# Performance work log

Hardware: AMD Instinct MI355X
Metric: run time of the kernel (lower is better)

Reference implementation:

```python
import jax, jax.numpy as jnp
import numpy as np

QMIN, QMAX = 0.0, 255.0  # uint8 activation quantization range


def _qlinear(x, w_q, b, s_in, zp_in, s_w):
    """zentorch_qlinear: quantize fp32 x to uint8, int8 weight, dequant output.

    x:   [M, K] fp32
    w_q: [N, K] int8 values (stored int32), symmetric (weight zp = 0)
    b:   [N] fp32
    s_in, zp_in: scalars (activation scale / zero point)
    s_w: [N] per-output-channel weight scales
    """
    zp = zp_in.astype(jnp.float32)
    q = jnp.clip(jnp.round(x / s_in) + zp, QMIN, QMAX)      # fake-quant uint8
    x_dq = (q - zp) * s_in                                   # dequantized activation
    w_dq = w_q.astype(jnp.float32) * s_w[:, None]            # [N, K] dequant weight
    return x_dq @ w_dq.T + b                                 # [M, N] fp32


def setup_inputs() -> dict:
    key = jax.random.key(0)
    k1, k2, k3, k4 = jax.random.split(key, 4)
    M, K, N = 8192, 4096, 4096
    inp = {
        "input": jax.random.normal(k1, (M, K), dtype=jnp.float32),
        "weights": jax.random.randint(k2, (N, K), -128, 128, dtype=jnp.int32),
        "biases": jax.random.normal(k3, (N,), dtype=jnp.float32) * 0.1,
        "input_scales": jnp.array([0.05], dtype=jnp.float32),
        "input_zero_points": jnp.array([128], dtype=jnp.int32),
        "weight_scales": jax.random.uniform(k4, (N,), dtype=jnp.float32, minval=0.001, maxval=0.01),
        "weight_zero_points": jnp.zeros((N,), dtype=jnp.int32),
        "output_dtype": 0,  # 0 -> float32
    }
    return inp


def reference(input, weights, biases, input_scales, input_zero_points,
              weight_scales, weight_zero_points, output_dtype):
    s_in = input_scales[0]
    zp_in = input_zero_points[0]
    x = _qlinear(input, weights, biases, s_in, zp_in, weight_scales)
    x = _qlinear(x, weights, biases, s_in, zp_in, weight_scales)
    x = _qlinear(x, weights, biases, s_in, zp_in, weight_scales)
    return x
```

## Files before the change

### kernel.cpp

```cpp
#include <hip/hip_runtime.h>
#include <stdint.h>

#define M_DIM 8192
#define K_DIM 4096
#define N_DIM 4096
#define KTILES (K_DIM / 64)

typedef __attribute__((ext_vector_type(4))) int i32x4;

__global__ void pack_w_kernel(const int* __restrict__ w, char* __restrict__ wp,
                              int* __restrict__ corr, const int* __restrict__ zpp) {
  __shared__ int red[256];
  const int n = blockIdx.x;
  const int t = threadIdx.x;
  const int4* row = (const int4*)(w + (size_t)n * K_DIM);
  int s = 0;
  int words[4];
#pragma unroll
  for (int u = 0; u < 4; ++u) {
    int4 v = row[t * 4 + u];
    s += v.x + v.y + v.z + v.w;
    words[u] = (v.x & 255) | ((v.y & 255) << 8) | ((v.z & 255) << 16) | (v.w << 24);
  }
  ((int4*)(wp + (size_t)n * K_DIM))[t] = make_int4(words[0], words[1], words[2], words[3]);
  red[t] = s;
  __syncthreads();
  for (int off = 128; off > 0; off >>= 1) {
    if (t < off) red[t] += red[t + off];
    __syncthreads();
  }
  if (t == 0) corr[n] = (128 - zpp[0]) * red[0];
}

__global__ void quant_in_kernel(const float* __restrict__ x, char* __restrict__ q,
                                const float* __restrict__ sp, const int* __restrict__ zpp) {
  const int i = blockIdx.x * blockDim.x + threadIdx.x;
  const float s = sp[0];
  const float zp = (float)zpp[0];
  float4 v = ((const float4*)x)[i];
  float t0 = fminf(fmaxf(rintf(v.x / s) + zp, 0.f), 255.f);
  float t1 = fminf(fmaxf(rintf(v.y / s) + zp, 0.f), 255.f);
  float t2 = fminf(fmaxf(rintf(v.z / s) + zp, 0.f), 255.f);
  float t3 = fminf(fmaxf(rintf(v.w / s) + zp, 0.f), 255.f);
  int b0 = (int)t0 - 128, b1 = (int)t1 - 128, b2 = (int)t2 - 128, b3 = (int)t3 - 128;
  ((int*)q)[i] = (b0 & 255) | ((b1 & 255) << 8) | ((b2 & 255) << 16) | (b3 << 24);
}

#define STAGE16(SRC, DST)                                                     \
  __builtin_amdgcn_global_load_lds(                                           \
      (const __attribute__((address_space(1))) void*)(SRC),                   \
      (__attribute__((address_space(3))) void*)(DST), 16, 0, 0)

#define RD(p) (*(const i32x4*)(p))

#define TILE(SLOT, KSTG, DO_NEXT)                                             \
  {                                                                           \
    const char* bufA_ = &lds[SLOT][0][0];                                     \
    char* nA_ = &lds[((SLOT) + 3) & 3][0][0];                                 \
    char* nB_ = &lds[((SLOT) + 3) & 3][1][0];                                 \
    i32x4 a1_[4];                                                             \
    _Pragma("unroll") for (int i_ = 0; i_ < 4; ++i_)                          \
        a1_[i_] = RD(bufA_ + aoff[4 + i_]);                                   \
    STAGE16(asrc0 + (size_t)(KSTG) * 64, nA_ + o0_);                          \
    STAGE16(asrc1 + (size_t)(KSTG) * 64, nA_ + o1_);                          \
    __builtin_amdgcn_s_setprio(1);                                            \
    _Pragma("unroll") for (int i_ = 0; i_ < 4; ++i_)                          \
        _Pragma("unroll") for (int j_ = 0; j_ < 4; ++j_)                      \
            acc[i_][j_] = __builtin_amdgcn_mfma_i32_16x16x64_i8(              \
                a0[i_], b0[j_], acc[i_][j_], 0, 0, 0);                        \
    __builtin_amdgcn_s_setprio(0);                                            \
    i32x4 ta_[4], tb_[4];                                                     \
    if (DO_NEXT) {                                                            \
      const char* xA_ = &lds[((SLOT) + 1) & 3][0][0];                         \
      const char* xB_ = &lds[((SLOT) + 1) & 3][1][0];                         \
      _Pragma("unroll") for (int i_ = 0; i_ < 4; ++i_)                        \
          ta_[i_] = RD(xA_ + aoff[i_]);                                       \
      _Pragma("unroll") for (int j_ = 0; j_ < 4; ++j_)                        \
          tb_[j_] = RD(xB_ + boff[j_]);                                       \
    }                                                                         \
    STAGE16(bsrc0 + (size_t)(KSTG) * 64, nB_ + o0_);                          \
    STAGE16(bsrc1 + (size_t)(KSTG) * 64, nB_ + o1_);                          \
    __builtin_amdgcn_s_setprio(1);                                            \
    _Pragma("unroll") for (int i_ = 0; i_ < 4; ++i_)                          \
        _Pragma("unroll") for (int j_ = 0; j_ < 4; ++j_)                      \
            acc[4 + i_][j_] = __builtin_amdgcn_mfma_i32_16x16x64_i8(          \
                a1_[i_], b0[j_], acc[4 + i_][j_], 0, 0, 0);                   \
    __builtin_amdgcn_s_setprio(0);                                            \
    asm volatile("s_waitcnt vmcnt(4)" ::: "memory");                          \
    __builtin_amdgcn_s_barrier();                                             \
    if (DO_NEXT) {                                                            \
      _Pragma("unroll") for (int i_ = 0; i_ < 4; ++i_) a0[i_] = ta_[i_];      \
      _Pragma("unroll") for (int j_ = 0; j_ < 4; ++j_) b0[j_] = tb_[j_];      \
    }                                                                         \
  }

template <int WRITE_Q>
__global__ __launch_bounds__(512, 2) void gemm_kernel(
    const char* __restrict__ qa, const char* __restrict__ wb,
    const int* __restrict__ corr, const float* __restrict__ swp,
    const float* __restrict__ bias, const float* __restrict__ sp,
    const int* __restrict__ zpp, char* __restrict__ outq, float* __restrict__ outf) {
  __shared__ __align__(16) char lds[4][2][16384];
  const int tid = threadIdx.x;
  const int lane = tid & 63;
  const int w = tid >> 6;
  const int wr = w >> 2;
  const int wc = w & 3;
  const int bid = blockIdx.x;
  const int bm = bid & 31;
  const int bn = bid >> 5;
  const char* abase = qa + (size_t)bm * 256 * K_DIM;
  const char* bbase = wb + (size_t)bn * 256 * K_DIM;

  const int o0_ = tid * 16;
  const int o1_ = 8192 + tid * 16;
  const int r0_ = o0_ >> 6, r1_ = o1_ >> 6;
  const int g0_ = ((o0_ >> 4) & 3) ^ ((r0_ >> 1) & 3);
  const int g1_ = ((o1_ >> 4) & 3) ^ ((r1_ >> 1) & 3);
  const char* asrc0 = abase + (size_t)r0_ * K_DIM + g0_ * 16;
  const char* asrc1 = abase + (size_t)r1_ * K_DIM + g1_ * 16;
  const char* bsrc0 = bbase + (size_t)r0_ * K_DIM + g0_ * 16;
  const char* bsrc1 = bbase + (size_t)r1_ * K_DIM + g1_ * 16;

  const int rr = lane & 15;
  const int g = lane >> 4;
  int aoff[8], boff[4];
#pragma unroll
  for (int i = 0; i < 8; ++i) {
    const int row = wr * 128 + i * 16 + rr;
    aoff[i] = (row << 6) + ((g ^ ((row >> 1) & 3)) << 4);
  }
#pragma unroll
  for (int j = 0; j < 4; ++j) {
    const int row = wc * 64 + j * 16 + rr;
    boff[j] = (row << 6) + ((g ^ ((row >> 1) & 3)) << 4);
  }

  i32x4 acc[8][4] = {};

  STAGE16(asrc0, &lds[0][0][o0_]); STAGE16(asrc1, &lds[0][0][o1_]);
  STAGE16(bsrc0, &lds[0][1][o0_]); STAGE16(bsrc1, &lds[0][1][o1_]);
  STAGE16(asrc0 + 64, &lds[1][0][o0_]); STAGE16(asrc1 + 64, &lds[1][0][o1_]);
  STAGE16(bsrc0 + 64, &lds[1][1][o0_]); STAGE16(bsrc1 + 64, &lds[1][1][o1_]);
  STAGE16(asrc0 + 128, &lds[2][0][o0_]); STAGE16(asrc1 + 128, &lds[2][0][o1_]);
  STAGE16(bsrc0 + 128, &lds[2][1][o0_]); STAGE16(bsrc1 + 128, &lds[2][1][o1_]);
  asm volatile("s_waitcnt vmcnt(4)" ::: "memory");
  __builtin_amdgcn_s_barrier();

  i32x4 a0[4], b0[4];
#pragma unroll
  for (int i = 0; i < 4; ++i) a0[i] = RD(&lds[0][0][0] + aoff[i]);
#pragma unroll
  for (int j = 0; j < 4; ++j) b0[j] = RD(&lds[0][1][0] + boff[j]);

  for (int tb = 0; tb < (KTILES - 4) / 4; ++tb) {
    const int t0 = tb * 4;
#pragma unroll
    for (int u = 0; u < 4; ++u) {
      TILE(u, t0 + u + 3, 1);
    }
  }
  TILE(0, KTILES - 1, 1);
  TILE(1, KTILES - 1, 1);
  TILE(2, KTILES - 1, 1);
  TILE(3, KTILES - 1, 0);
  asm volatile("s_waitcnt vmcnt(0)" ::: "memory");

  const float s = sp[0];
  const float zpf = (float)zpp[0];
  const int m0 = bm * 256 + wr * 128 + (lane >> 4) * 4;
  const int n0 = bn * 256 + wc * 64 + (lane & 15);
#pragma unroll
  for (int j = 0; j < 4; ++j) {
    const int n = n0 + j * 16;
    const int cr = corr[n];
    const float fs = s * swp[n];
    const float bb = bias[n];
#pragma unroll
    for (int i = 0; i < 8; ++i) {
#pragma unroll
      for (int q = 0; q < 4; ++q) {
        const int m = m0 + i * 16 + q;
        float val = fs * (float)(acc[i][j][q] + cr) + bb;
        if (WRITE_Q) {
          float tq = fminf(fmaxf(rintf(val / s) + zpf, 0.f), 255.f);
          outq[(size_t)m * N_DIM + n] = (char)((int)tq - 128);
        } else {
          outf[(size_t)m * N_DIM + n] = val;
        }
      }
    }
  }
}

extern "C" void kernel_launch(void* const* d_in, const int* in_sizes, int n_in,
                              void* d_out, int out_size, void* d_ws, size_t ws_size,
                              hipStream_t stream) {
  const float* x = (const float*)d_in[0];
  const int* wq = (const int*)d_in[1];
  const float* bias = (const float*)d_in[2];
  const float* s_in = (const float*)d_in[3];
  const int* zp_in = (const int*)d_in[4];
  const float* s_w = (const float*)d_in[5];
  float* out = (float*)d_out;

  const size_t WP_BYTES = (size_t)N_DIM * K_DIM;
  const size_t Q_BYTES = (size_t)M_DIM * K_DIM;
  char* ws = (char*)d_ws;
  char* wp = ws;
  char* q1 = ws + WP_BYTES;
  char* q2 = q1 + Q_BYTES;
  int* corr = (int*)(q2 + Q_BYTES);
  const size_t NEEDED = WP_BYTES + 2 * Q_BYTES + (size_t)N_DIM * sizeof(int);
  if (ws_size < NEEDED) return;

  pack_w_kernel<<<N_DIM, 256, 0, stream>>>(wq, wp, corr, zp_in);
  quant_in_kernel<<<(M_DIM * K_DIM / 4) / 256, 256, 0, stream>>>(x, q1, s_in, zp_in);

  dim3 grid((M_DIM / 256) * (N_DIM / 256));
  dim3 blk(512);
  gemm_kernel<1><<<grid, blk, 0, stream>>>(q1, wp, corr, s_w, bias, s_in, zp_in, q2, nullptr);
  gemm_kernel<1><<<grid, blk, 0, stream>>>(q2, wp, corr, s_w, bias, s_in, zp_in, q1, nullptr);
  gemm_kernel<0><<<grid, blk, 0, stream>>>(q1, wp, corr, s_w, bias, s_in, zp_in, nullptr, out);
}
```

Measured before the change: 451.7 us.

## Switch int8 GEMM to 32x32x32 MFMA tiles with direct register prefetch

Replaces the 16x16x64 int8 MFMA with the 32x32x32 variant. Each wave's 128x64 output tile now takes 4x2 accumulator blocks of 16 ints, and fragment offsets, the LDS read pattern and epilogue indexing are recomputed for that layout. Prefetched next-tile fragments now load straight into a0/b0 instead of temporaries, and sched_barriers pin the ordering. The larger MFMA reads fewer LDS fragments per unit of math, which cuts LDS traffic and instruction count. In exchange it changes the epilogue store pattern and register pressure.

Result: slower. 479.7 us (+6.2%).

```diff
diff --git a/kernel.cpp b/kernel.cpp
--- a/kernel.cpp
+++ b/kernel.cpp
@@ -7,6 +7,7 @@
 #define KTILES (K_DIM / 64)
 
 typedef __attribute__((ext_vector_type(4))) int i32x4;
+typedef __attribute__((ext_vector_type(16))) int i32x16;
 
 __global__ void pack_w_kernel(const int* __restrict__ w, char* __restrict__ wp,
                               int* __restrict__ corr, const int* __restrict__ zpp) {
@@ -56,42 +57,42 @@
 #define TILE(SLOT, KSTG, DO_NEXT)                                             \
   {                                                                           \
     const char* bufA_ = &lds[SLOT][0][0];                                     \
+    const char* bufB_ = &lds[SLOT][1][0];                                     \
     char* nA_ = &lds[((SLOT) + 3) & 3][0][0];                                 \
     char* nB_ = &lds[((SLOT) + 3) & 3][1][0];                                 \
-    i32x4 a1_[4];                                                             \
+    i32x4 a1_[4], b1_[2];                                                     \
     _Pragma("unroll") for (int i_ = 0; i_ < 4; ++i_)                          \
         a1_[i_] = RD(bufA_ + aoff[4 + i_]);                                   \
+    _Pragma("unroll") for (int j_ = 0; j_ < 2; ++j_)                          \
+        b1_[j_] = RD(bufB_ + boff[2 + j_]);                                   \
     STAGE16(asrc0 + (size_t)(KSTG) * 64, nA_ + o0_);                          \
     STAGE16(asrc1 + (size_t)(KSTG) * 64, nA_ + o1_);                          \
+    __builtin_amdgcn_sched_barrier(0);                                        \
     __builtin_amdgcn_s_setprio(1);                                            \
     _Pragma("unroll") for (int i_ = 0; i_ < 4; ++i_)                          \
-        _Pragma("unroll") for (int j_ = 0; j_ < 4; ++j_)                      \
-            acc[i_][j_] = __builtin_amdgcn_mfma_i32_16x16x64_i8(              \
+        _Pragma("unroll") for (int j_ = 0; j_ < 2; ++j_)                      \
+            acc[i_][j_] = __builtin_amdgcn_mfma_i32_32x32x32_i8(              \
                 a0[i_], b0[j_], acc[i_][j_], 0, 0, 0);                        \
     __builtin_amdgcn_s_setprio(0);                                            \
-    i32x4 ta_[4], tb_[4];                                                     \
     if (DO_NEXT) {                                                            \
       const char* xA_ = &lds[((SLOT) + 1) & 3][0][0];                         \
       const char* xB_ = &lds[((SLOT) + 1) & 3][1][0];                         \
       _Pragma("unroll") for (int i_ = 0; i_ < 4; ++i_)                        \
-          ta_[i_] = RD(xA_ + aoff[i_]);                                       \
-      _Pragma("unroll") for (int j_ = 0; j_ < 4; ++j_)                        \
-          tb_[j_] = RD(xB_ + boff[j_]);                                       \
+          a0[i_] = RD(xA_ + aoff[i_]);                                        \
+      _Pragma("unroll") for (int j_ = 0; j_ < 2; ++j_)                        \
+          b0[j_] = RD(xB_ + boff[j_]);                                        \
     }                                                                         \
     STAGE16(bsrc0 + (size_t)(KSTG) * 64, nB_ + o0_);                          \
     STAGE16(bsrc1 + (size_t)(KSTG) * 64, nB_ + o1_);                          \
+    __builtin_amdgcn_sched_barrier(0);                                        \
     __builtin_amdgcn_s_setprio(1);                                            \
     _Pragma("unroll") for (int i_ = 0; i_ < 4; ++i_)                          \
-        _Pragma("unroll") for (int j_ = 0; j_ < 4; ++j_)                      \
-            acc[4 + i_][j_] = __builtin_amdgcn_mfma_i32_16x16x64_i8(          \
-                a1_[i_], b0[j_], acc[4 + i_][j_], 0, 0, 0);                   \
+        _Pragma("unroll") for (int j_ = 0; j_ < 2; ++j_)                      \
+            acc[i_][j_] = __builtin_amdgcn_mfma_i32_32x32x32_i8(              \
+                a1_[i_], b1_[j_], acc[i_][j_], 0, 0, 0);                      \
     __builtin_amdgcn_s_setprio(0);                                            \
     asm volatile("s_waitcnt vmcnt(4)" ::: "memory");                          \
     __builtin_amdgcn_s_barrier();                                             \
-    if (DO_NEXT) {                                                            \
-      _Pragma("unroll") for (int i_ = 0; i_ < 4; ++i_) a0[i_] = ta_[i_];      \
-      _Pragma("unroll") for (int j_ = 0; j_ < 4; ++j_) b0[j_] = tb_[j_];      \
-    }                                                                         \
   }
 
 template <int WRITE_Q>
@@ -122,21 +123,26 @@
   const char* bsrc0 = bbase + (size_t)r0_ * K_DIM + g0_ * 16;
   const char* bsrc1 = bbase + (size_t)r1_ * K_DIM + g1_ * 16;
 
-  const int rr = lane & 15;
-  const int g = lane >> 4;
+  const int r32 = lane & 31;
+  const int kh = lane >> 5;
   int aoff[8], boff[4];
 #pragma unroll
-  for (int i = 0; i < 8; ++i) {
-    const int row = wr * 128 + i * 16 + rr;
-    aoff[i] = (row << 6) + ((g ^ ((row >> 1) & 3)) << 4);
-  }
-#pragma unroll
-  for (int j = 0; j < 4; ++j) {
-    const int row = wc * 64 + j * 16 + rr;
-    boff[j] = (row << 6) + ((g ^ ((row >> 1) & 3)) << 4);
-  }
-
-  i32x4 acc[8][4] = {};
+  for (int ks = 0; ks < 2; ++ks) {
+#pragma unroll
+    for (int mt = 0; mt < 4; ++mt) {
+      const int row = wr * 128 + mt * 32 + r32;
+      const int slot = ks * 2 + kh;
+      aoff[ks * 4 + mt] = (row << 6) + ((slot ^ ((row >> 1) & 3)) << 4);
+    }
+#pragma unroll
+    for (int nt = 0; nt < 2; ++nt) {
+      const int row = wc * 64 + nt * 32 + r32;
+      const int slot = ks * 2 + kh;
+      boff[ks * 2 + nt] = (row << 6) + ((slot ^ ((row >> 1) & 3)) << 4);
+    }
+  }
+
+  i32x16 acc[4][2] = {};
 
   STAGE16(asrc0, &lds[0][0][o0_]); STAGE16(asrc1, &lds[0][0][o1_]);
   STAGE16(bsrc0, &lds[0][1][o0_]); STAGE16(bsrc1, &lds[0][1][o1_]);
@@ -147,11 +153,11 @@
   asm volatile("s_waitcnt vmcnt(4)" ::: "memory");
   __builtin_amdgcn_s_barrier();
 
-  i32x4 a0[4], b0[4];
+  i32x4 a0[4], b0[2];
 #pragma unroll
   for (int i = 0; i < 4; ++i) a0[i] = RD(&lds[0][0][0] + aoff[i]);
 #pragma unroll
-  for (int j = 0; j < 4; ++j) b0[j] = RD(&lds[0][1][0] + boff[j]);
+  for (int j = 0; j < 2; ++j) b0[j] = RD(&lds[0][1][0] + boff[j]);
 
   for (int tb = 0; tb < (KTILES - 4) / 4; ++tb) {
     const int t0 = tb * 4;
@@ -168,20 +174,20 @@
 
   const float s = sp[0];
   const float zpf = (float)zpp[0];
-  const int m0 = bm * 256 + wr * 128 + (lane >> 4) * 4;
-  const int n0 = bn * 256 + wc * 64 + (lane & 15);
-#pragma unroll
-  for (int j = 0; j < 4; ++j) {
-    const int n = n0 + j * 16;
+  const int lm = kh * 4;
+#pragma unroll
+  for (int nt = 0; nt < 2; ++nt) {
+    const int n = bn * 256 + wc * 64 + nt * 32 + r32;
     const int cr = corr[n];
     const float fs = s * swp[n];
     const float bb = bias[n];
 #pragma unroll
-    for (int i = 0; i < 8; ++i) {
-#pragma unroll
-      for (int q = 0; q < 4; ++q) {
-        const int m = m0 + i * 16 + q;
-        float val = fs * (float)(acc[i][j][q] + cr) + bb;
+    for (int mt = 0; mt < 4; ++mt) {
+      const int mb = bm * 256 + wr * 128 + mt * 32 + lm;
+#pragma unroll
+      for (int r = 0; r < 16; ++r) {
+        const int m = mb + (r & 3) + 8 * (r >> 2);
+        float val = fs * (float)(acc[mt][nt][r] + cr) + bb;
         if (WRITE_Q) {
           float tq = fminf(fmaxf(rintf(val / s) + zpf, 0.f), 255.f);
           outq[(size_t)m * N_DIM + n] = (char)((int)tq - 128);
```

## Load A operand directly from global into registers, stage only B through LDS

Applied to the files above, without the earlier changes.

Removes the LDS staging buffers for the activation (A) tile. Each wave now reads its A fragments straight from global memory into registers, one k-tile ahead, and only the weight (B) tile still goes through the 4-slot LDS ring. This halves LDS usage and cuts LDS write/read traffic for A. In exchange, the four waves sharing the same A rows each fetch them separately, so global/L2 traffic for A rises and the accesses are less coalesced. The vmcnt(2) wait also forces the next-tile A loads to finish within one tile of MFMA work, which can expose global memory latency.

After: 1.169 ms. 2.59x slower.

```diff
diff --git a/kernel.cpp b/kernel.cpp
--- a/kernel.cpp
+++ b/kernel.cpp
@@ -53,44 +53,37 @@
 
 #define RD(p) (*(const i32x4*)(p))
 
-#define TILE(SLOT, KSTG, DO_NEXT)                                             \
+#define TILE(SLOT, KA, KB, DO_NEXT)                                           \
   {                                                                           \
-    const char* bufA_ = &lds[SLOT][0][0];                                     \
-    char* nA_ = &lds[((SLOT) + 3) & 3][0][0];                                 \
-    char* nB_ = &lds[((SLOT) + 3) & 3][1][0];                                 \
-    i32x4 a1_[4];                                                             \
-    _Pragma("unroll") for (int i_ = 0; i_ < 4; ++i_)                          \
-        a1_[i_] = RD(bufA_ + aoff[4 + i_]);                                   \
-    STAGE16(asrc0 + (size_t)(KSTG) * 64, nA_ + o0_);                          \
-    STAGE16(asrc1 + (size_t)(KSTG) * 64, nA_ + o1_);                          \
+    i32x4 an_[8];                                                             \
+    if (DO_NEXT) {                                                            \
+      _Pragma("unroll") for (int i_ = 0; i_ < 8; ++i_)                        \
+          an_[i_] = RD(abase + (KA) + aoffg[i_]);                             \
+    }                                                                         \
+    STAGE16(bsrc0 + (size_t)(KB), &ldsB[((SLOT) + 3) & 3][o0_]);              \
+    STAGE16(bsrc1 + (size_t)(KB), &ldsB[((SLOT) + 3) & 3][o1_]);              \
     __builtin_amdgcn_s_setprio(1);                                            \
     _Pragma("unroll") for (int i_ = 0; i_ < 4; ++i_)                          \
         _Pragma("unroll") for (int j_ = 0; j_ < 4; ++j_)                      \
             acc[i_][j_] = __builtin_amdgcn_mfma_i32_16x16x64_i8(              \
-                a0[i_], b0[j_], acc[i_][j_], 0, 0, 0);                        \
+                ac[i_], bc[j_], acc[i_][j_], 0, 0, 0);                        \
     __builtin_amdgcn_s_setprio(0);                                            \
-    i32x4 ta_[4], tb_[4];                                                     \
+    i32x4 bn_[4];                                                             \
     if (DO_NEXT) {                                                            \
-      const char* xA_ = &lds[((SLOT) + 1) & 3][0][0];                         \
-      const char* xB_ = &lds[((SLOT) + 1) & 3][1][0];                         \
-      _Pragma("unroll") for (int i_ = 0; i_ < 4; ++i_)                        \
-          ta_[i_] = RD(xA_ + aoff[i_]);                                       \
       _Pragma("unroll") for (int j_ = 0; j_ < 4; ++j_)                        \
-          tb_[j_] = RD(xB_ + boff[j_]);                                       \
+          bn_[j_] = RD(&ldsB[((SLOT) + 1) & 3][0] + boff[j_]);                \
     }                                                                         \
-    STAGE16(bsrc0 + (size_t)(KSTG) * 64, nB_ + o0_);                          \
-    STAGE16(bsrc1 + (size_t)(KSTG) * 64, nB_ + o1_);                          \
     __builtin_amdgcn_s_setprio(1);                                            \
     _Pragma("unroll") for (int i_ = 0; i_ < 4; ++i_)                          \
         _Pragma("unroll") for (int j_ = 0; j_ < 4; ++j_)                      \
             acc[4 + i_][j_] = __builtin_amdgcn_mfma_i32_16x16x64_i8(          \
-                a1_[i_], b0[j_], acc[4 + i_][j_], 0, 0, 0);                   \
+                ac[4 + i_], bc[j_], acc[4 + i_][j_], 0, 0, 0);                \
     __builtin_amdgcn_s_setprio(0);                                            \
-    asm volatile("s_waitcnt vmcnt(4)" ::: "memory");                          \
+    asm volatile("s_waitcnt vmcnt(2)" ::: "memory");                          \
     __builtin_amdgcn_s_barrier();                                             \
     if (DO_NEXT) {                                                            \
-      _Pragma("unroll") for (int i_ = 0; i_ < 4; ++i_) a0[i_] = ta_[i_];      \
-      _Pragma("unroll") for (int j_ = 0; j_ < 4; ++j_) b0[j_] = tb_[j_];      \
+      _Pragma("unroll") for (int i_ = 0; i_ < 8; ++i_) ac[i_] = an_[i_];      \
+      _Pragma("unroll") for (int j_ = 0; j_ < 4; ++j_) bc[j_] = bn_[j_];      \
     }                                                                         \
   }
 
@@ -100,7 +93,7 @@
     const int* __restrict__ corr, const float* __restrict__ swp,
     const float* __restrict__ bias, const float* __restrict__ sp,
     const int* __restrict__ zpp, char* __restrict__ outq, float* __restrict__ outf) {
-  __shared__ __align__(16) char lds[4][2][16384];
+  __shared__ __align__(16) char ldsB[4][16384];
   const int tid = threadIdx.x;
   const int lane = tid & 63;
   const int w = tid >> 6;
@@ -117,19 +110,18 @@
   const int r0_ = o0_ >> 6, r1_ = o1_ >> 6;
   const int g0_ = ((o0_ >> 4) & 3) ^ ((r0_ >> 1) & 3);
   const int g1_ = ((o1_ >> 4) & 3) ^ ((r1_ >> 1) & 3);
-  const char* asrc0 = abase + (size_t)r0_ * K_DIM + g0_ * 16;
-  const char* asrc1 = abase + (size_t)r1_ * K_DIM + g1_ * 16;
   const char* bsrc0 = bbase + (size_t)r0_ * K_DIM + g0_ * 16;
   const char* bsrc1 = bbase + (size_t)r1_ * K_DIM + g1_ * 16;
 
   const int rr = lane & 15;
   const int g = lane >> 4;
-  int aoff[8], boff[4];
+  int aoffg[8];
 #pragma unroll
   for (int i = 0; i < 8; ++i) {
     const int row = wr * 128 + i * 16 + rr;
-    aoff[i] = (row << 6) + ((g ^ ((row >> 1) & 3)) << 4);
-  }
+    aoffg[i] = row * K_DIM + g * 16;
+  }
+  int boff[4];
 #pragma unroll
   for (int j = 0; j < 4; ++j) {
     const int row = wc * 64 + j * 16 + rr;
@@ -138,32 +130,27 @@
 
   i32x4 acc[8][4] = {};
 
-  STAGE16(asrc0, &lds[0][0][o0_]); STAGE16(asrc1, &lds[0][0][o1_]);
-  STAGE16(bsrc0, &lds[0][1][o0_]); STAGE16(bsrc1, &lds[0][1][o1_]);
-  STAGE16(asrc0 + 64, &lds[1][0][o0_]); STAGE16(asrc1 + 64, &lds[1][0][o1_]);
-  STAGE16(bsrc0 + 64, &lds[1][1][o0_]); STAGE16(bsrc1 + 64, &lds[1][1][o1_]);
-  STAGE16(asrc0 + 128, &lds[2][0][o0_]); STAGE16(asrc1 + 128, &lds[2][0][o1_]);
-  STAGE16(bsrc0 + 128, &lds[2][1][o0_]); STAGE16(bsrc1 + 128, &lds[2][1][o1_]);
-  asm volatile("s_waitcnt vmcnt(4)" ::: "memory");
+  STAGE16(bsrc0, &ldsB[0][o0_]); STAGE16(bsrc1, &ldsB[0][o1_]);
+  STAGE16(bsrc0 + 64, &ldsB[1][o0_]); STAGE16(bsrc1 + 64, &ldsB[1][o1_]);
+  i32x4 ac[8], bc[4];
+#pragma unroll
+  for (int i = 0; i < 8; ++i) ac[i] = RD(abase + aoffg[i]);
+  STAGE16(bsrc0 + 128, &ldsB[2][o0_]); STAGE16(bsrc1 + 128, &ldsB[2][o1_]);
+  asm volatile("s_waitcnt vmcnt(2)" ::: "memory");
   __builtin_amdgcn_s_barrier();
-
-  i32x4 a0[4], b0[4];
-#pragma unroll
-  for (int i = 0; i < 4; ++i) a0[i] = RD(&lds[0][0][0] + aoff[i]);
-#pragma unroll
-  for (int j = 0; j < 4; ++j) b0[j] = RD(&lds[0][1][0] + boff[j]);
-
-  for (int tb = 0; tb < (KTILES - 4) / 4; ++tb) {
-    const int t0 = tb * 4;
+#pragma unroll
+  for (int j = 0; j < 4; ++j) bc[j] = RD(&ldsB[0][0] + boff[j]);
+
+  for (int tb = 0; tb < KTILES / 4; ++tb) {
 #pragma unroll
     for (int u = 0; u < 4; ++u) {
-      TILE(u, t0 + u + 3, 1);
+      const int t = tb * 4 + u;
+      const int ka = (t + 1 < KTILES ? t + 1 : KTILES - 1) * 64;
+      const int kb = (t + 3 < KTILES ? t + 3 : KTILES - 1) * 64;
+      const int last = (t == KTILES - 1);
+      TILE(u, ka, kb, !last);
     }
   }
-  TILE(0, KTILES - 1, 1);
-  TILE(1, KTILES - 1, 1);
-  TILE(2, KTILES - 1, 1);
-  TILE(3, KTILES - 1, 0);
   asm volatile("s_waitcnt vmcnt(0)" ::: "memory");
 
   const float s = sp[0];
```

## Stagger MFMA/LDS schedules across wave groups and permute B rows for vector epilogue stores

Applied to the files above, without the earlier changes.

The two wave groups now run differently ordered tile bodies (TILEA/TILEB) with sched_barriers, so one group's LDS reads and global-to-LDS staging overlap the other's MFMA bursts. B rows are loaded in a permuted order, so each lane's four accumulator columns map to four consecutive output columns. The epilogue can then do vectorised int4/float4 parameter loads and packed 4-byte or 16-byte stores instead of scalar scattered writes. It adds code size and relies on the row permutation staying consistent with the correction and scale indexing.

Result: slower. 466.0 us (+3.2%).

```diff
diff --git a/kernel.cpp b/kernel.cpp
--- a/kernel.cpp
+++ b/kernel.cpp
@@ -53,7 +53,23 @@
 
 #define RD(p) (*(const i32x4*)(p))
 
-#define TILE(SLOT, KSTG, DO_NEXT)                                             \
+#define MFMA_C0                                                               \
+  __builtin_amdgcn_s_setprio(1);                                              \
+  _Pragma("unroll") for (int i_ = 0; i_ < 4; ++i_)                            \
+      _Pragma("unroll") for (int j_ = 0; j_ < 4; ++j_)                        \
+          acc[i_][j_] = __builtin_amdgcn_mfma_i32_16x16x64_i8(                \
+              a0[i_], b0[j_], acc[i_][j_], 0, 0, 0);                          \
+  __builtin_amdgcn_s_setprio(0);
+
+#define MFMA_C1(A1)                                                           \
+  __builtin_amdgcn_s_setprio(1);                                              \
+  _Pragma("unroll") for (int i_ = 0; i_ < 4; ++i_)                            \
+      _Pragma("unroll") for (int j_ = 0; j_ < 4; ++j_)                        \
+          acc[4 + i_][j_] = __builtin_amdgcn_mfma_i32_16x16x64_i8(            \
+              A1[i_], b0[j_], acc[4 + i_][j_], 0, 0, 0);                      \
+  __builtin_amdgcn_s_setprio(0);
+
+#define TILEA(SLOT, KSTG, DO_NEXT)                                            \
   {                                                                           \
     const char* bufA_ = &lds[SLOT][0][0];                                     \
     char* nA_ = &lds[((SLOT) + 3) & 3][0][0];                                 \
@@ -63,12 +79,8 @@
         a1_[i_] = RD(bufA_ + aoff[4 + i_]);                                   \
     STAGE16(asrc0 + (size_t)(KSTG) * 64, nA_ + o0_);                          \
     STAGE16(asrc1 + (size_t)(KSTG) * 64, nA_ + o1_);                          \
-    __builtin_amdgcn_s_setprio(1);                                            \
-    _Pragma("unroll") for (int i_ = 0; i_ < 4; ++i_)                          \
-        _Pragma("unroll") for (int j_ = 0; j_ < 4; ++j_)                      \
-            acc[i_][j_] = __builtin_amdgcn_mfma_i32_16x16x64_i8(              \
-                a0[i_], b0[j_], acc[i_][j_], 0, 0, 0);                        \
-    __builtin_amdgcn_s_setprio(0);                                            \
+    __builtin_amdgcn_sched_barrier(0);                                        \
+    MFMA_C0                                                                   \
     i32x4 ta_[4], tb_[4];                                                     \
     if (DO_NEXT) {                                                            \
       const char* xA_ = &lds[((SLOT) + 1) & 3][0][0];                         \
@@ -80,18 +92,43 @@
     }                                                                         \
     STAGE16(bsrc0 + (size_t)(KSTG) * 64, nB_ + o0_);                          \
     STAGE16(bsrc1 + (size_t)(KSTG) * 64, nB_ + o1_);                          \
-    __builtin_amdgcn_s_setprio(1);                                            \
-    _Pragma("unroll") for (int i_ = 0; i_ < 4; ++i_)                          \
-        _Pragma("unroll") for (int j_ = 0; j_ < 4; ++j_)                      \
-            acc[4 + i_][j_] = __builtin_amdgcn_mfma_i32_16x16x64_i8(          \
-                a1_[i_], b0[j_], acc[4 + i_][j_], 0, 0, 0);                   \
-    __builtin_amdgcn_s_setprio(0);                                            \
+    __builtin_amdgcn_sched_barrier(0);                                        \
+    MFMA_C1(a1_)                                                              \
     asm volatile("s_waitcnt vmcnt(4)" ::: "memory");                          \
     __builtin_amdgcn_s_barrier();                                             \
     if (DO_NEXT) {                                                            \
       _Pragma("unroll") for (int i_ = 0; i_ < 4; ++i_) a0[i_] = ta_[i_];      \
       _Pragma("unroll") for (int j_ = 0; j_ < 4; ++j_) b0[j_] = tb_[j_];      \
     }                                                                         \
+  }
+
+#define TILEB(SLOT, KSTG, DO_NEXT)                                            \
+  {                                                                           \
+    const char* bufA_ = &lds[SLOT][0][0];                                     \
+    char* nA_ = &lds[((SLOT) + 3) & 3][0][0];                                 \
+    char* nB_ = &lds[((SLOT) + 3) & 3][1][0];                                 \
+    MFMA_C0                                                                   \
+    __builtin_amdgcn_sched_barrier(0);                                        \
+    i32x4 a1_[4];                                                             \
+    _Pragma("unroll") for (int i_ = 0; i_ < 4; ++i_)                          \
+        a1_[i_] = RD(bufA_ + aoff[4 + i_]);                                   \
+    STAGE16(asrc0 + (size_t)(KSTG) * 64, nA_ + o0_);                          \
+    STAGE16(asrc1 + (size_t)(KSTG) * 64, nA_ + o1_);                          \
+    __builtin_amdgcn_sched_barrier(0);                                        \
+    MFMA_C1(a1_)                                                              \
+    __builtin_amdgcn_sched_barrier(0);                                        \
+    if (DO_NEXT) {                                                            \
+      const char* xA_ = &lds[((SLOT) + 1) & 3][0][0];                         \
+      const char* xB_ = &lds[((SLOT) + 1) & 3][1][0];                         \
+      _Pragma("unroll") for (int i_ = 0; i_ < 4; ++i_)                        \
+          a0[i_] = RD(xA_ + aoff[i_]);                                        \
+      _Pragma("unroll") for (int j_ = 0; j_ < 4; ++j_)                        \
+          b0[j_] = RD(xB_ + boff[j_]);                                        \
+    }                                                                         \
+    STAGE16(bsrc0 + (size_t)(KSTG) * 64, nB_ + o0_);                          \
+    STAGE16(bsrc1 + (size_t)(KSTG) * 64, nB_ + o1_);                          \
+    asm volatile("s_waitcnt vmcnt(4)" ::: "memory");                          \
+    __builtin_amdgcn_s_barrier();                                             \
   }
 
 template <int WRITE_Q>
@@ -106,6 +143,7 @@
   const int w = tid >> 6;
   const int wr = w >> 2;
   const int wc = w & 3;
+  const int wgrp = (w >> 2) & 1;
   const int bid = blockIdx.x;
   const int bm = bid & 31;
   const int bn = bid >> 5;
@@ -119,8 +157,10 @@
   const int g1_ = ((o1_ >> 4) & 3) ^ ((r1_ >> 1) & 3);
   const char* asrc0 = abase + (size_t)r0_ * K_DIM + g0_ * 16;
   const char* asrc1 = abase + (size_t)r1_ * K_DIM + g1_ * 16;
-  const char* bsrc0 = bbase + (size_t)r0_ * K_DIM + g0_ * 16;
-  const char* bsrc1 = bbase + (size_t)r1_ * K_DIM + g1_ * 16;
+  const int p0_ = (r0_ & ~63) + 4 * (r0_ & 15) + ((r0_ >> 4) & 3);
+  const int p1_ = (r1_ & ~63) + 4 * (r1_ & 15) + ((r1_ >> 4) & 3);
+  const char* bsrc0 = bbase + (size_t)p0_ * K_DIM + g0_ * 16;
+  const char* bsrc1 = bbase + (size_t)p1_ * K_DIM + g1_ * 16;
 
   const int rr = lane & 15;
   const int g = lane >> 4;
@@ -153,41 +193,58 @@
 #pragma unroll
   for (int j = 0; j < 4; ++j) b0[j] = RD(&lds[0][1][0] + boff[j]);
 
-  for (int tb = 0; tb < (KTILES - 4) / 4; ++tb) {
-    const int t0 = tb * 4;
-#pragma unroll
-    for (int u = 0; u < 4; ++u) {
-      TILE(u, t0 + u + 3, 1);
+  if (wgrp == 0) {
+    for (int tb = 0; tb < (KTILES - 4) / 4; ++tb) {
+      const int t0 = tb * 4;
+#pragma unroll
+      for (int u = 0; u < 4; ++u) { TILEA(u, t0 + u + 3, 1); }
     }
-  }
-  TILE(0, KTILES - 1, 1);
-  TILE(1, KTILES - 1, 1);
-  TILE(2, KTILES - 1, 1);
-  TILE(3, KTILES - 1, 0);
+    TILEA(0, KTILES - 1, 1);
+    TILEA(1, KTILES - 1, 1);
+    TILEA(2, KTILES - 1, 1);
+    TILEA(3, KTILES - 1, 0);
+  } else {
+    for (int tb = 0; tb < (KTILES - 4) / 4; ++tb) {
+      const int t0 = tb * 4;
+#pragma unroll
+      for (int u = 0; u < 4; ++u) { TILEB(u, t0 + u + 3, 1); }
+    }
+    TILEB(0, KTILES - 1, 1);
+    TILEB(1, KTILES - 1, 1);
+    TILEB(2, KTILES - 1, 1);
+    TILEB(3, KTILES - 1, 0);
+  }
   asm volatile("s_waitcnt vmcnt(0)" ::: "memory");
 
   const float s = sp[0];
   const float zpf = (float)zpp[0];
   const int m0 = bm * 256 + wr * 128 + (lane >> 4) * 4;
-  const int n0 = bn * 256 + wc * 64 + (lane & 15);
-#pragma unroll
-  for (int j = 0; j < 4; ++j) {
-    const int n = n0 + j * 16;
-    const int cr = corr[n];
-    const float fs = s * swp[n];
-    const float bb = bias[n];
-#pragma unroll
-    for (int i = 0; i < 8; ++i) {
-#pragma unroll
-      for (int q = 0; q < 4; ++q) {
-        const int m = m0 + i * 16 + q;
-        float val = fs * (float)(acc[i][j][q] + cr) + bb;
-        if (WRITE_Q) {
-          float tq = fminf(fmaxf(rintf(val / s) + zpf, 0.f), 255.f);
-          outq[(size_t)m * N_DIM + n] = (char)((int)tq - 128);
-        } else {
-          outf[(size_t)m * N_DIM + n] = val;
-        }
+  const int nb4 = bn * 256 + wc * 64 + ((lane & 15) << 2);
+  const int4 cr4 = *(const int4*)(corr + nb4);
+  const float4 sw4 = *(const float4*)(swp + nb4);
+  const float4 bb4 = *(const float4*)(bias + nb4);
+  const float fs0 = s * sw4.x, fs1 = s * sw4.y, fs2 = s * sw4.z, fs3 = s * sw4.w;
+#pragma unroll
+  for (int i = 0; i < 8; ++i) {
+#pragma unroll
+    for (int q = 0; q < 4; ++q) {
+      const int m = m0 + i * 16 + q;
+      const float v0 = fs0 * (float)(acc[i][0][q] + cr4.x) + bb4.x;
+      const float v1 = fs1 * (float)(acc[i][1][q] + cr4.y) + bb4.y;
+      const float v2 = fs2 * (float)(acc[i][2][q] + cr4.z) + bb4.z;
+      const float v3 = fs3 * (float)(acc[i][3][q] + cr4.w) + bb4.w;
+      if (WRITE_Q) {
+        const int b0i = (int)fminf(fmaxf(rintf(v0 / s) + zpf, 0.f), 255.f) - 128;
+        const int b1i = (int)fminf(fmaxf(rintf(v1 / s) + zpf, 0.f), 255.f) - 128;
+        const int b2i = (int)fminf(fmaxf(rintf(v2 / s) + zpf, 0.f), 255.f) - 128;
+        const int b3i = (int)fminf(fmaxf(rintf(v3 / s) + zpf, 0.f), 255.f) - 128;
+        const uint32_t pk = (uint32_t)(b0i & 255) | ((uint32_t)(b1i & 255) << 8) |
+                            ((uint32_t)(b2i & 255) << 16) | ((uint32_t)b3i << 24);
+        *(uint32_t*)(outq + (size_t)m * N_DIM + nb4) = pk;
+      } else {
+        float4 o4;
+        o4.x = v0; o4.y = v1; o4.z = v2; o4.w = v3;
+        *(float4*)(outf + (size_t)m * N_DIM + nb4) = o4;
       }
     }
   }
```
